# Kernel optimization log

Hardware: AMD Instinct MI355X
Metric: run time of the kernel (lower is better)

## Reference

```python
import jax, jax.numpy as jnp
import numpy as np

E = 8        # num_experts
K = 2        # top_k
CAP = 512    # hard-coded capacity in MoELayer
H = 2048     # hidden_dim
F = 8192     # ffn_dim


def setup_inputs() -> dict:
    key = jax.random.key(0)
    ks = jax.random.split(key, 6)
    inp = {
        "hidden_states": jax.random.normal(ks[0], (2, 1024, H), jnp.float32),
        "router_w": jax.random.normal(ks[1], (E, H), jnp.float32) * (0.01 / np.sqrt(H)),
        "w1": jax.random.normal(ks[2], (F, H), jnp.float32) * (1.0 / np.sqrt(H)),
        "b1": jax.random.normal(ks[3], (F,), jnp.float32) * 0.01,
        "w2": jax.random.normal(ks[4], (H, F), jnp.float32) * (1.0 / np.sqrt(F)),
        "b2": jax.random.normal(ks[5], (H,), jnp.float32) * 0.01,
    }
    return inp


def reference(hidden_states, router_w, w1, b1, w2, b2):
    orig_shape = hidden_states.shape
    x = hidden_states.reshape(-1, H)          # [N, H]
    N = x.shape[0]

    # --- Router: softmax then top-k ---
    logits = x @ router_w.T                   # [N, E]
    probs = jax.nn.softmax(logits, axis=-1)
    top_p, top_i = jax.lax.top_k(probs, K)    # [N, K]

    # --- Capacity-based permute (slot-major order: all slot-0 tokens, then slot-1,
    # matching the torch loop over top_k slots within each expert) ---
    expert_flat = top_i.T.reshape(-1)         # [K*N] int
    probs_flat = top_p.T.reshape(-1)          # [K*N]
    token_idx = jnp.tile(jnp.arange(N), K)    # [K*N]

    onehot = (expert_flat[:, None] == jnp.arange(E)[None, :]).astype(jnp.int32)  # [K*N, E]
    # position of each routed token within its expert's queue
    pos = jnp.take_along_axis(jnp.cumsum(onehot, axis=0), expert_flat[:, None], axis=1)[:, 0] - 1
    keep = pos < CAP                          # deterministic truncation at capacity
    dest = expert_flat * CAP + pos            # slot in [E*CAP] dispatch buffer
    dest_m = jnp.where(keep, dest, E * CAP)   # out-of-range -> dropped by scatter

    buf = jnp.zeros((E * CAP, H), x.dtype).at[dest_m].set(x[token_idx], mode='drop')

    # --- Shared expert FFN (all2all is identity on one device) ---
    h = jax.nn.gelu(buf @ w1.T + b1, approximate=False) @ w2.T + b2  # [E*CAP, H]

    # --- Weighted combine (scatter-add back to token positions) ---
    gathered = jnp.where(keep[:, None], h[jnp.where(keep, dest, 0)], 0.0) * probs_flat[:, None]
    out = jnp.zeros_like(x).at[token_idx].add(gathered)
    return out.reshape(orig_shape)
```

## Files before the change

### kernel.cpp

```cpp
#include <hip/hip_runtime.h>

#define HD 2048
#define FD 8192
#define NE 8
#define CAP 512

typedef __attribute__((ext_vector_type(4))) float f32x4;
typedef __attribute__((ext_vector_type(8))) __bf16 bf16x8;

__device__ __forceinline__ void gload_lds16(const __bf16* g, __bf16* l) {
    __builtin_amdgcn_global_load_lds(
        (const __attribute__((address_space(1))) void*)g,
        (__attribute__((address_space(3))) void*)l, 16, 0, 0);
}

__global__ __launch_bounds__(256) void cvt_k(const float* __restrict__ src,
                                             __bf16* __restrict__ dst, int n8) {
    int i = blockIdx.x * 256 + threadIdx.x;
    if (i >= n8) return;
    const float* s = src + (size_t)i * 8;
    f32x4 a = *(const f32x4*)s;
    f32x4 b = *(const f32x4*)(s + 4);
    bf16x8 o;
    o[0] = (__bf16)a[0]; o[1] = (__bf16)a[1]; o[2] = (__bf16)a[2]; o[3] = (__bf16)a[3];
    o[4] = (__bf16)b[0]; o[5] = (__bf16)b[1]; o[6] = (__bf16)b[2]; o[7] = (__bf16)b[3];
    *(bf16x8*)(dst + (size_t)i * 8) = o;
}

__global__ __launch_bounds__(256) void router_k(const float* __restrict__ x,
                                                const float* __restrict__ rw,
                                                int2* __restrict__ experts,
                                                float2* __restrict__ probs, int Ntok) {
    int wave = threadIdx.x >> 6, lane = threadIdx.x & 63;
    int n = blockIdx.x * 4 + wave;
    if (n >= Ntok) return;
    const float* xr = x + (size_t)n * HD;
    double acc[NE];
#pragma unroll
    for (int e = 0; e < NE; e++) acc[e] = 0.0;
    for (int i = 0; i < HD / 64; i++) {
        float xv = xr[lane + 64 * i];
#pragma unroll
        for (int e = 0; e < NE; e++)
            acc[e] += (double)xv * (double)rw[e * HD + lane + 64 * i];
    }
#pragma unroll
    for (int e = 0; e < NE; e++) {
        double v = acc[e];
        for (int off = 32; off > 0; off >>= 1) v += __shfl_xor(v, off);
        acc[e] = v;
    }
    if (lane == 0) {
        double mx = acc[0];
#pragma unroll
        for (int e = 1; e < NE; e++) mx = acc[e] > mx ? acc[e] : mx;
        double s = 0.0;
#pragma unroll
        for (int e = 0; e < NE; e++) s += exp(acc[e] - mx);
        float pf[NE];
#pragma unroll
        for (int e = 0; e < NE; e++) pf[e] = (float)(exp(acc[e] - mx) / s);
        int e0 = 0; float b0 = pf[0];
#pragma unroll
        for (int e = 1; e < NE; e++) if (pf[e] > b0) { b0 = pf[e]; e0 = e; }
        int e1 = -1; float b1 = -1.0f;
#pragma unroll
        for (int e = 0; e < NE; e++) if (e != e0 && pf[e] > b1) { b1 = pf[e]; e1 = e; }
        experts[n] = make_int2(e0, e1);
        probs[n] = make_float2(b0, b1);
    }
}

__global__ __launch_bounds__(256) void scan_k(const int2* __restrict__ experts,
                                              int* __restrict__ dest,
                                              int* __restrict__ slot_token, int Ntok) {
    __shared__ int cnts[256][NE];
    int tid = threadIdx.x;
    for (int i = tid; i < NE * CAP; i += 256) slot_token[i] = -1;
    int per = (2 * Ntok) / 256;
    int base = tid * per;
    int c[NE];
#pragma unroll
    for (int e = 0; e < NE; e++) c[e] = 0;
    int eloc[16];
    for (int i = 0; i < per; i++) {
        int j = base + i;
        int t = j & (Ntok - 1);
        int2 ex = experts[t];
        int e = (j >= Ntok) ? ex.y : ex.x;
        eloc[i] = e;
        c[e]++;
    }
#pragma unroll
    for (int e = 0; e < NE; e++) cnts[tid][e] = c[e];
    __syncthreads();
    if (tid < NE) {
        int run = 0;
        for (int t2 = 0; t2 < 256; t2++) { int v = cnts[t2][tid]; cnts[t2][tid] = run; run += v; }
    }
    __syncthreads();
    int b[NE];
#pragma unroll
    for (int e = 0; e < NE; e++) b[e] = cnts[tid][e];
    for (int i = 0; i < per; i++) {
        int j = base + i;
        int t = j & (Ntok - 1);
        int e = eloc[i];
        int pos = b[e]++;
        if (pos < CAP) {
            int d = e * CAP + pos;
            dest[j] = d;
            slot_token[d] = t;
        } else {
            dest[j] = -1;
        }
    }
}

__global__ __launch_bounds__(256) void dispatch_k(const float* __restrict__ x,
                                                  const int* __restrict__ slot_token,
                                                  __bf16* __restrict__ buf) {
    int slot = blockIdx.x;
    int tok = slot_token[slot];
    int idx = threadIdx.x * 8;
    __bf16* drow = buf + (size_t)slot * HD + idx;
    if (tok >= 0) {
        const float* srow = x + (size_t)tok * HD + idx;
        f32x4 a = *(const f32x4*)srow;
        f32x4 b = *(const f32x4*)(srow + 4);
        bf16x8 o;
        o[0] = (__bf16)a[0]; o[1] = (__bf16)a[1]; o[2] = (__bf16)a[2]; o[3] = (__bf16)a[3];
        o[4] = (__bf16)b[0]; o[5] = (__bf16)b[1]; o[6] = (__bf16)b[2]; o[7] = (__bf16)b[3];
        *(bf16x8*)drow = o;
    } else {
        f32x4 z = 0;
        *(f32x4*)drow = z;
    }
}

__device__ inline float gelu_exact(float v) {
    return 0.5f * v * (1.0f + erff(v * 0.70710678118654752f));
}

template <int EPI>
__global__ __launch_bounds__(256) void gemm_nt(const __bf16* __restrict__ A,
                                               const __bf16* __restrict__ B,
                                               const float* __restrict__ bias,
                                               void* __restrict__ Cout,
                                               int M, int N, int K) {
    __shared__ __align__(16) __bf16 As[128 * 64];
    __shared__ __align__(16) __bf16 Bs[128 * 64];
    int m0 = blockIdx.y * 128, n0 = blockIdx.x * 128;
    int tid = threadIdx.x;
    int lane = tid & 63;
    int wave = tid >> 6;
    int wr = wave >> 1, wc = wave & 1;
    int lrow = lane & 15, lk = (lane >> 4) * 8;

    int sr = tid >> 3;
    int sc = (tid & 7) * 8;
    const __bf16* Ag = A + (size_t)(m0 + sr) * K + sc;
    const __bf16* Bg = B + (size_t)(n0 + sr) * K + sc;
    __bf16* Al = As + sr * 64 + sc;
    __bf16* Bl = Bs + sr * 64 + sc;

    f32x4 acc[4][4];
#pragma unroll
    for (int m = 0; m < 4; m++)
#pragma unroll
        for (int n = 0; n < 4; n++) acc[m][n] = 0;

    for (int kt = 0; kt < K; kt += 64) {
#pragma unroll
        for (int i = 0; i < 4; i++) {
            gload_lds16(Ag + (size_t)(i * 32) * K + kt, Al + i * 2048);
            gload_lds16(Bg + (size_t)(i * 32) * K + kt, Bl + i * 2048);
        }
        __syncthreads();
#pragma unroll
        for (int kk = 0; kk < 2; kk++) {
            bf16x8 af[4], bfr[4];
            int kb = kk * 32 + lk;
#pragma unroll
            for (int m = 0; m < 4; m++)
                af[m] = *(const bf16x8*)&As[(wr * 64 + m * 16 + lrow) * 64 + kb];
#pragma unroll
            for (int n = 0; n < 4; n++)
                bfr[n] = *(const bf16x8*)&Bs[(wc * 64 + n * 16 + lrow) * 64 + kb];
#pragma unroll
            for (int m = 0; m < 4; m++)
#pragma unroll
                for (int n = 0; n < 4; n++)
                    acc[m][n] = __builtin_amdgcn_mfma_f32_16x16x32_bf16(
                        af[m], bfr[n], acc[m][n], 0, 0, 0);
        }
        __syncthreads();
    }

    int col_base = n0 + wc * 64;
    int row_base = m0 + wr * 64 + (lane >> 4) * 4;
#pragma unroll
    for (int n = 0; n < 4; n++) {
        int col = col_base + n * 16 + lrow;
        float bv = bias[col];
#pragma unroll
        for (int m = 0; m < 4; m++) {
            int row0 = row_base + m * 16;
#pragma unroll
            for (int r = 0; r < 4; r++) {
                float v = acc[m][n][r] + bv;
                if (EPI == 0) {
                    ((__bf16*)Cout)[(size_t)(row0 + r) * N + col] = (__bf16)gelu_exact(v);
                } else {
                    ((float*)Cout)[(size_t)(row0 + r) * N + col] = v;
                }
            }
        }
    }
}

__global__ __launch_bounds__(256) void combine_k(const float* __restrict__ h2,
                                                 const int* __restrict__ dest,
                                                 const float2* __restrict__ probs,
                                                 float* __restrict__ out, int Ntok) {
    int t = blockIdx.x;
    int d0 = dest[t], d1 = dest[Ntok + t];
    float2 p = probs[t];
    int idx = threadIdx.x * 8;
    f32x4 o0 = 0, o1 = 0;
    if (d0 >= 0) {
        const float* r = h2 + (size_t)d0 * HD + idx;
        o0 += p.x * (*(const f32x4*)r);
        o1 += p.x * (*(const f32x4*)(r + 4));
    }
    if (d1 >= 0) {
        const float* r = h2 + (size_t)d1 * HD + idx;
        o0 += p.y * (*(const f32x4*)r);
        o1 += p.y * (*(const f32x4*)(r + 4));
    }
    float* w = out + (size_t)t * HD + idx;
    *(f32x4*)w = o0;
    *(f32x4*)(w + 4) = o1;
}

extern "C" void kernel_launch(void* const* d_in, const int* in_sizes, int n_in,
                              void* d_out, int out_size, void* d_ws, size_t ws_size,
                              hipStream_t stream) {
    const float* x  = (const float*)d_in[0];
    const float* rw = (const float*)d_in[1];
    const float* w1 = (const float*)d_in[2];
    const float* b1 = (const float*)d_in[3];
    const float* w2 = (const float*)d_in[4];
    const float* b2 = (const float*)d_in[5];
    float* out = (float*)d_out;
    int Ntok = in_sizes[0] / HD;

    char* ws = (char*)d_ws;
    __bf16* w1b = (__bf16*)ws;            ws += (size_t)FD * HD * 2;
    __bf16* w2b = (__bf16*)ws;            ws += (size_t)HD * FD * 2;
    __bf16* buf = (__bf16*)ws;            ws += (size_t)NE * CAP * HD * 2;
    __bf16* h1  = (__bf16*)ws;            ws += (size_t)NE * CAP * FD * 2;
    float*  h2  = (float*)ws;             ws += (size_t)NE * CAP * HD * 4;
    int2*   experts = (int2*)ws;          ws += (size_t)Ntok * 8;
    float2* probsb  = (float2*)ws;        ws += (size_t)Ntok * 8;
    int*    dest    = (int*)ws;           ws += (size_t)2 * Ntok * 4;
    int*    slot_token = (int*)ws;        ws += (size_t)NE * CAP * 4;

    int n8 = FD * HD / 8;
    cvt_k<<<n8 / 256, 256, 0, stream>>>(w1, w1b, n8);
    cvt_k<<<n8 / 256, 256, 0, stream>>>(w2, w2b, n8);
    router_k<<<Ntok / 4, 256, 0, stream>>>(x, rw, experts, probsb, Ntok);
    scan_k<<<1, 256, 0, stream>>>(experts, dest, slot_token, Ntok);
    dispatch_k<<<NE * CAP, 256, 0, stream>>>(x, slot_token, buf);
    gemm_nt<0><<<dim3(FD / 128, (NE * CAP) / 128), 256, 0, stream>>>(
        buf, w1b, b1, (void*)h1, NE * CAP, FD, HD);
    gemm_nt<1><<<dim3(HD / 128, (NE * CAP) / 128), 256, 0, stream>>>(
        h1, w2b, b2, (void*)h2, NE * CAP, HD, FD);
    combine_k<<<Ntok, 256, 0, stream>>>(h2, dest, probsb, out, Ntok);
}
```

Before: 611.4 us.

## Replace GEMM with 8-wave double-buffered, swizzled LDS pipeline with larger tiles

Both FFN GEMMs move to a new 512-thread kernel with larger output tiles (256x256 for the first, 128x256 for the second). It double-buffers A and B in LDS, issues the next tiles' global-to-LDS loads in stages across the four MFMA sub-steps, and waits with explicit vmcnt counts instead of full syncthreads. Row reads are XOR-swizzled to avoid LDS bank conflicts, and s_setprio is raised around the MFMA bursts. The goal is to hide memory latency and raise MFMA utilisation, at the cost of more registers, more LDS per block and fewer blocks for the smaller second GEMM (64 blocks).

Measured after the change: 526.7 us. 13.8% less time.

```diff
diff --git a/kernel.cpp b/kernel.cpp
--- a/kernel.cpp
+++ b/kernel.cpp
@@ -13,6 +13,8 @@
         (const __attribute__((address_space(1))) void*)g,
         (__attribute__((address_space(3))) void*)l, 16, 0, 0);
 }
+__device__ __forceinline__ void waitv4() { asm volatile("s_waitcnt vmcnt(4)" ::: "memory"); }
+__device__ __forceinline__ void waitv0() { asm volatile("s_waitcnt vmcnt(0)" ::: "memory"); }
 
 __global__ __launch_bounds__(256) void cvt_k(const float* __restrict__ src,
                                              __bf16* __restrict__ dst, int n8) {
@@ -142,73 +144,127 @@
     return 0.5f * v * (1.0f + erff(v * 0.70710678118654752f));
 }
 
-template <int EPI>
-__global__ __launch_bounds__(256) void gemm_nt(const __bf16* __restrict__ A,
-                                               const __bf16* __restrict__ B,
-                                               const float* __restrict__ bias,
-                                               void* __restrict__ Cout,
-                                               int M, int N, int K) {
-    __shared__ __align__(16) __bf16 As[128 * 64];
-    __shared__ __align__(16) __bf16 Bs[128 * 64];
-    int m0 = blockIdx.y * 128, n0 = blockIdx.x * 128;
+template <int EPI, int BM, int ALOADS, int QM>
+__global__ __launch_bounds__(512) void gemm8p(const __bf16* __restrict__ A,
+                                              const __bf16* __restrict__ B,
+                                              const float* __restrict__ bias,
+                                              void* __restrict__ Cout,
+                                              int N, int K) {
+    constexpr int MREP = 4 * QM;
+    __shared__ __align__(16) __bf16 As[2][BM * 64];
+    __shared__ __align__(16) __bf16 Bs[2][256 * 64];
+    int m0 = blockIdx.y * BM, n0 = blockIdx.x * 256;
     int tid = threadIdx.x;
-    int lane = tid & 63;
-    int wave = tid >> 6;
-    int wr = wave >> 1, wc = wave & 1;
-    int lrow = lane & 15, lk = (lane >> 4) * 8;
+    int lane = tid & 63, wave = tid >> 6;
+    int wr = wave >> 2, wc = wave & 3;
+    int lrow = lane & 15, l16 = lane >> 4;
+    int NT = K >> 6;
 
     int sr = tid >> 3;
-    int sc = (tid & 7) * 8;
-    const __bf16* Ag = A + (size_t)(m0 + sr) * K + sc;
-    const __bf16* Bg = B + (size_t)(n0 + sr) * K + sc;
-    __bf16* Al = As + sr * 64 + sc;
-    __bf16* Bl = Bs + sr * 64 + sc;
-
-    f32x4 acc[4][4];
-#pragma unroll
-    for (int m = 0; m < 4; m++)
+    int c8 = tid & 7;
+    int csw = (c8 ^ (sr & 7)) * 8;
+    const __bf16* Ag = A + (size_t)(m0 + sr) * K + csw;
+    const __bf16* Bg = B + (size_t)(n0 + sr) * K + csw;
+    int ldst = sr * 64 + c8 * 8;
+
+    int rch0 = ((0 + l16) ^ (lrow & 7)) * 8;
+    int rch1 = ((4 + l16) ^ (lrow & 7)) * 8;
+
+    f32x4 acc[MREP][4];
+#pragma unroll
+    for (int m = 0; m < MREP; m++)
 #pragma unroll
         for (int n = 0; n < 4; n++) acc[m][n] = 0;
 
-    for (int kt = 0; kt < K; kt += 64) {
-#pragma unroll
-        for (int i = 0; i < 4; i++) {
-            gload_lds16(Ag + (size_t)(i * 32) * K + kt, Al + i * 2048);
-            gload_lds16(Bg + (size_t)(i * 32) * K + kt, Bl + i * 2048);
+#pragma unroll
+    for (int i = 0; i < ALOADS; i++)
+        gload_lds16(Ag + (size_t)(i * 64) * K, &As[0][ldst + i * 4096]);
+#pragma unroll
+    for (int i = 0; i < 4; i++)
+        gload_lds16(Bg + (size_t)(i * 64) * K, &Bs[0][ldst + i * 4096]);
+#pragma unroll
+    for (int i = 0; i < 4; i++)
+        gload_lds16(Bg + (size_t)(i * 64) * K + 64, &Bs[1][ldst + i * 4096]);
+    waitv4();
+    __builtin_amdgcn_s_barrier();
+
+    for (int t = 0; t < NT; ++t) {
+        int p = t & 1;
+        const __bf16* Asl = As[p];
+        const __bf16* Bsl = Bs[p];
+        bf16x8 bf[4][2];
+#pragma unroll
+        for (int q = 0; q < 4; ++q) {
+            bf16x8 af[QM][2];
+#pragma unroll
+            for (int j = 0; j < QM; j++) {
+                int row = (wr * (BM / 2) + (q * QM + j) * 16 + lrow) * 64;
+                af[j][0] = *(const bf16x8*)&Asl[row + rch0];
+                af[j][1] = *(const bf16x8*)&Asl[row + rch1];
+            }
+            if (q == 0) {
+#pragma unroll
+                for (int n = 0; n < 4; n++) {
+                    int row = (wc * 64 + n * 16 + lrow) * 64;
+                    bf[n][0] = *(const bf16x8*)&Bsl[row + rch0];
+                    bf[n][1] = *(const bf16x8*)&Bsl[row + rch1];
+                }
+                if (t + 1 < NT) {
+                    gload_lds16(Ag + (size_t)(t + 1) * 64, &As[(t + 1) & 1][ldst]);
+                    gload_lds16(Ag + (size_t)64 * K + (size_t)(t + 1) * 64,
+                                &As[(t + 1) & 1][ldst + 4096]);
+                }
+            } else if (q == 1) {
+                if (ALOADS == 4 && t + 1 < NT) {
+                    gload_lds16(Ag + (size_t)128 * K + (size_t)(t + 1) * 64,
+                                &As[(t + 1) & 1][ldst + 8192]);
+                    gload_lds16(Ag + (size_t)192 * K + (size_t)(t + 1) * 64,
+                                &As[(t + 1) & 1][ldst + 12288]);
+                }
+            } else if (q == 2) {
+                if (t + 2 < NT) {
+                    gload_lds16(Bg + (size_t)(t + 2) * 64, &Bs[t & 1][ldst]);
+                    gload_lds16(Bg + (size_t)64 * K + (size_t)(t + 2) * 64,
+                                &Bs[t & 1][ldst + 4096]);
+                }
+            } else {
+                if (t + 2 < NT) {
+                    gload_lds16(Bg + (size_t)128 * K + (size_t)(t + 2) * 64,
+                                &Bs[t & 1][ldst + 8192]);
+                    gload_lds16(Bg + (size_t)192 * K + (size_t)(t + 2) * 64,
+                                &Bs[t & 1][ldst + 12288]);
+                }
+            }
+            __builtin_amdgcn_s_barrier();
+            __builtin_amdgcn_s_setprio(1);
+#pragma unroll
+            for (int j = 0; j < QM; j++)
+#pragma unroll
+                for (int n = 0; n < 4; n++)
+#pragma unroll
+                    for (int kk = 0; kk < 2; kk++)
+                        acc[q * QM + j][n] = __builtin_amdgcn_mfma_f32_16x16x32_bf16(
+                            af[j][kk], bf[n][kk], acc[q * QM + j][n], 0, 0, 0);
+            __builtin_amdgcn_s_setprio(0);
+            if (q == 3) {
+                if (t + 2 < NT) waitv4(); else waitv0();
+            }
+            __builtin_amdgcn_s_barrier();
         }
-        __syncthreads();
-#pragma unroll
-        for (int kk = 0; kk < 2; kk++) {
-            bf16x8 af[4], bfr[4];
-            int kb = kk * 32 + lk;
-#pragma unroll
-            for (int m = 0; m < 4; m++)
-                af[m] = *(const bf16x8*)&As[(wr * 64 + m * 16 + lrow) * 64 + kb];
-#pragma unroll
-            for (int n = 0; n < 4; n++)
-                bfr[n] = *(const bf16x8*)&Bs[(wc * 64 + n * 16 + lrow) * 64 + kb];
-#pragma unroll
-            for (int m = 0; m < 4; m++)
-#pragma unroll
-                for (int n = 0; n < 4; n++)
-                    acc[m][n] = __builtin_amdgcn_mfma_f32_16x16x32_bf16(
-                        af[m], bfr[n], acc[m][n], 0, 0, 0);
-        }
-        __syncthreads();
     }
 
     int col_base = n0 + wc * 64;
-    int row_base = m0 + wr * 64 + (lane >> 4) * 4;
+    int row_base0 = m0 + wr * (BM / 2) + l16 * 4;
 #pragma unroll
     for (int n = 0; n < 4; n++) {
         int col = col_base + n * 16 + lrow;
         float bv = bias[col];
 #pragma unroll
-        for (int m = 0; m < 4; m++) {
-            int row0 = row_base + m * 16;
+        for (int mf = 0; mf < MREP; mf++) {
+            int row0 = row_base0 + mf * 16;
 #pragma unroll
             for (int r = 0; r < 4; r++) {
-                float v = acc[m][n][r] + bv;
+                float v = acc[mf][n][r] + bv;
                 if (EPI == 0) {
                     ((__bf16*)Cout)[(size_t)(row0 + r) * N + col] = (__bf16)gelu_exact(v);
                 } else {
@@ -272,9 +328,9 @@
     router_k<<<Ntok / 4, 256, 0, stream>>>(x, rw, experts, probsb, Ntok);
     scan_k<<<1, 256, 0, stream>>>(experts, dest, slot_token, Ntok);
     dispatch_k<<<NE * CAP, 256, 0, stream>>>(x, slot_token, buf);
-    gemm_nt<0><<<dim3(FD / 128, (NE * CAP) / 128), 256, 0, stream>>>(
-        buf, w1b, b1, (void*)h1, NE * CAP, FD, HD);
-    gemm_nt<1><<<dim3(HD / 128, (NE * CAP) / 128), 256, 0, stream>>>(
-        h1, w2b, b2, (void*)h2, NE * CAP, HD, FD);
+    gemm8p<0, 256, 4, 2><<<dim3(FD / 256, (NE * CAP) / 256), 512, 0, stream>>>(
+        buf, w1b, b1, (void*)h1, FD, HD);
+    gemm8p<1, 128, 2, 1><<<dim3(HD / 256, (NE * CAP) / 128), 512, 0, stream>>>(
+        h1, w2b, b2, (void*)h2, HD, FD);
     combine_k<<<Ntok, 256, 0, stream>>>(h2, dest, probsb, out, Ntok);
 }
```
